# Performance work log

Hardware: AMD Instinct MI355X
Metric: run time of the kernel (lower is better)

Reference implementation:

```python
import jax, jax.numpy as jnp
import numpy as np

N = 10000      # nodes
E = 160000     # edges
IN = 256       # input feature dim
HID = 128      # hidden per head
H = 4          # heads (all layers)
EMB = 128      # dim_embedding (last-layer out per head)
SLOPE = 0.2    # leaky_relu negative slope in attention


def _gat_layer(h, src, dst, W, al, ar, b, residual, apply_act):
    """DGL-style GATConv (no dropout). h: [N, F_in], W: [F_in, H*D], al/ar/b: [H, D]."""
    n = h.shape[0]
    heads, d = al.shape
    feat = (h @ W).reshape(n, heads, d)                 # [N, H, D]
    el = jnp.sum(feat * al, axis=-1)                    # [N, H]
    er = jnp.sum(feat * ar, axis=-1)                    # [N, H]
    e = jax.nn.leaky_relu(el[src] + er[dst], SLOPE)     # [E, H]
    # edge softmax over incoming edges of dst (numerically stable)
    m = jax.ops.segment_max(e, dst, num_segments=n)
    m = jnp.where(jnp.isfinite(m), m, 0.0)              # empty segments -> 0
    ex = jnp.exp(e - m[dst])
    den = jax.ops.segment_sum(ex, dst, num_segments=n)
    alpha = ex / jnp.maximum(den[dst], 1e-9)            # [E, H]
    rst = jax.ops.segment_sum(alpha[:, :, None] * feat[src], dst, num_segments=n)  # [N, H, D]
    if residual:
        rst = rst + h.reshape(n, heads, d)              # identity residual (dims match)
    rst = rst + b
    return jax.nn.elu(rst) if apply_act else rst


def setup_inputs() -> dict:
    key = jax.random.key(0)
    ks = jax.random.split(key, 24)
    def p(k, shape, scale):
        return (jax.random.normal(k, shape, jnp.float32) * scale)
    inp = {
        'x': jax.random.normal(ks[0], (N, IN), jnp.float32),
        'src': jax.random.randint(ks[1], (E,), 0, N, dtype=jnp.int32).astype(jnp.int64),
        'dst': jax.random.randint(ks[2], (E,), 0, N, dtype=jnp.int32).astype(jnp.int64),
        # layer 0: in=IN, out=HID per head
        'W0': p(ks[3], (IN, H * HID), 1.0 / np.sqrt(IN)),
        'al0': p(ks[4], (H, HID), 0.1), 'ar0': p(ks[5], (H, HID), 0.1),
        'b0': p(ks[6], (H, HID), 0.02),
        # layer 1: in=H*HID=512, out=HID per head, residual
        'W1': p(ks[7], (H * HID, H * HID), 1.0 / np.sqrt(H * HID)),
        'al1': p(ks[8], (H, HID), 0.1), 'ar1': p(ks[9], (H, HID), 0.1),
        'b1': p(ks[10], (H, HID), 0.02),
        # layer 2: in=H*HID=512, out=EMB per head, residual, no activation
        'W2': p(ks[11], (H * HID, H * EMB), 1.0 / np.sqrt(H * HID)),
        'al2': p(ks[12], (H, EMB), 0.1), 'ar2': p(ks[13], (H, EMB), 0.1),
        'b2': p(ks[14], (H, EMB), 0.02),
        # MLP predictor: 2*EMB -> EMB -> EMB//2 -> 1
        'Wm0': p(ks[15], (2 * EMB, EMB), 1.0 / np.sqrt(2 * EMB)), 'bm0': p(ks[16], (EMB,), 0.02),
        'Wm1': p(ks[17], (EMB, EMB // 2), 1.0 / np.sqrt(EMB)), 'bm1': p(ks[18], (EMB // 2,), 0.02),
        'Wm2': p(ks[19], (EMB // 2, 1), 1.0 / np.sqrt(EMB // 2)), 'bm2': p(ks[20], (1,), 0.02),
    }
    return inp


def reference(x, src, dst, W0, al0, ar0, b0, W1, al1, ar1, b1, W2, al2, ar2, b2,
              Wm0, bm0, Wm1, bm1, Wm2, bm2):
    # GAT encoder
    h = _gat_layer(x, src, dst, W0, al0, ar0, b0, residual=False, apply_act=True).reshape(N, -1)
    h = _gat_layer(h, src, dst, W1, al1, ar1, b1, residual=True, apply_act=True).reshape(N, -1)
    h = _gat_layer(h, src, dst, W2, al2, ar2, b2, residual=True, apply_act=False).mean(axis=1)  # [N, EMB]
    # link predictor over all graph edges
    emb = jnp.concatenate([h[src], h[dst]], axis=1)     # [E, 2*EMB]
    z = jax.nn.relu(emb @ Wm0 + bm0)
    z = jax.nn.relu(z @ Wm1 + bm1)
    return jax.nn.sigmoid(z @ Wm2 + bm2)                # [E, 1]
```

## Files before the change

kernel.cpp:

```cpp
#include <hip/hip_runtime.h>
#include <hip/hip_bf16.h>
#include <math.h>

constexpr int kN = 10000;
constexpr int kE = 160000;
constexpr float kSlope = 0.2f;

typedef short v8s __attribute__((ext_vector_type(8)));
typedef float f32x4 __attribute__((ext_vector_type(4)));
typedef unsigned short ushort_t;

__device__ __forceinline__ float lrelu(float x) { return x > 0.f ? x : kSlope * x; }
__device__ __forceinline__ float elu_f(float x) { return x > 0.f ? x : (__expf(x) - 1.f); }
__device__ __forceinline__ float b2f(ushort_t u) {
    return __uint_as_float(((unsigned)u) << 16);
}
__device__ __forceinline__ float bl(unsigned u) { return __uint_as_float(u << 16); }
__device__ __forceinline__ float bh(unsigned u) { return __uint_as_float(u & 0xffff0000u); }
__device__ __forceinline__ ushort_t f2b(float f) {
    unsigned u = __float_as_uint(f);
    return (ushort_t)((u + 0x7FFFu + ((u >> 16) & 1u)) >> 16);
}
__device__ __forceinline__ void gload16(const void* g, void* l) {
    __builtin_amdgcn_global_load_lds(
        (const __attribute__((address_space(1))) void*)g,
        (__attribute__((address_space(3))) void*)l, 16, 0, 0);
}

__global__ void detect_zero(const void* __restrict__ x, const void* __restrict__ dsti,
                            int* __restrict__ flags, int* __restrict__ deg) {
    if (blockIdx.x == 0) {
        __shared__ int sb[2];
        int tid = threadIdx.x;
        if (tid == 0) { sb[0] = 0; sb[1] = 0; }
        __syncthreads();
        const ushort_t* xb = (const ushort_t*)x;
        int big = 0;
        for (int i = tid; i < 4096; i += 256) {
            float v = b2f(xb[i]);
            if (!(fabsf(v) <= 1e4f)) big = 1;
        }
        const int* d32 = (const int*)dsti;
        int hi = 0;
        for (int i = tid; i < 4096; i += 256) hi |= d32[2 * i + 1];
        if (big) atomicOr(&sb[0], 1);
        if (hi)  atomicOr(&sb[1], 1);
        __syncthreads();
        if (tid == 0) { flags[0] = sb[0]; flags[1] = sb[1] ? 0 : 1; }
    } else {
        int i = (blockIdx.x - 1) * 256 + threadIdx.x;
        if (i < 2 * kN) deg[i] = 0;
    }
}

struct PrepArgs {
    const void* sm[13];
    const void* W0; const void* W1; const void* W2; const void* Wm0; const void* Wm1;
    const void* X; const void* srcIn; const void* dstIn;
    float* smallb;
    ushort_t* W0T; ushort_t* W1T; ushort_t* W2T; ushort_t* PQT; ushort_t* Wm1T;
    ushort_t* Xb;
    int* nsrc; int* ndst; int* deg;
    const int* flags;
};
constexpr int kPrepTotal = 4865 + 131072 + 262144 + 262144 + 32768 + 8192 + 2560000 + 320000;

__global__ void prep_all(PrepArgs a) {
    int i = blockIdx.x * 256 + threadIdx.x;
    if (i >= kPrepTotal) return;
    const int f32in = a.flags[0];
    auto cv = [&](const void* p, int idx) -> ushort_t {
        return f32in ? f2b(((const float*)p)[idx]) : ((const ushort_t*)p)[idx];
    };
    if (i < 4865) {
        int seg, offi;
        if (i < 4608)      { seg = i >> 9; offi = i & 511; }
        else if (i < 4736) { seg = 9;  offi = i - 4608; }
        else if (i < 4800) { seg = 10; offi = i - 4736; }
        else if (i < 4864) { seg = 11; offi = i - 4800; }
        else               { seg = 12; offi = 0; }
        a.smallb[i] = f32in ? ((const float*)a.sm[seg])[offi]
                            : b2f(((const ushort_t*)a.sm[seg])[offi]);
        return;
    }
    i -= 4865;
    if (i < 131072) {
        int n = i >> 8, k = i & 255;
        a.W0T[i] = cv(a.W0, k * 512 + n);
        return;
    }
    i -= 131072;
    if (i < 262144) {
        int n = i >> 9, k = i & 511;
        a.W1T[i] = cv(a.W1, k * 512 + n);
        return;
    }
    i -= 262144;
    if (i < 262144) {
        int n = i >> 9, k = i & 511;
        a.W2T[i] = cv(a.W2, k * 512 + n);
        return;
    }
    i -= 262144;
    if (i < 32768) {
        int n = i >> 7, k = i & 127;
        a.PQT[i] = cv(a.Wm0, (k + ((n < 128) ? 0 : 128)) * 128 + (n & 127));
        return;
    }
    i -= 32768;
    if (i < 8192) {
        int n = i >> 7, k = i & 127;
        a.Wm1T[i] = cv(a.Wm1, k * 64 + n);
        return;
    }
    i -= 8192;
    if (i < 2560000) {
        if (f32in) a.Xb[i] = f2b(((const float*)a.X)[i]);
        return;
    }
    i -= 2560000;
    {
        const void* in = (i < kE) ? a.srcIn : a.dstIn;
        int j = (i < kE) ? i : i - kE;
        int v = a.flags[1] ? (int)((const long long*)in)[j] : ((const int*)in)[j];
        v = ((unsigned)v < (unsigned)kN) ? v : 0;
        if (i < kE) a.nsrc[j] = v;
        else { a.ndst[j] = v; atomicAdd(&a.deg[v], 1); }
    }
}

__global__ __launch_bounds__(1024) void scan_off(const int* __restrict__ deg,
                                                 int* __restrict__ off, int n) {
    __shared__ int s[1024];
    int tid = threadIdx.x;
    int per = (n + 1023) >> 10;
    int base = tid * per;
    int sum = 0;
    for (int i = 0; i < per; ++i) { int j = base + i; if (j < n) sum += deg[j]; }
    s[tid] = sum;
    __syncthreads();
    for (int d = 1; d < 1024; d <<= 1) {
        int v = (tid >= d) ? s[tid - d] : 0;
        __syncthreads();
        s[tid] += v;
        __syncthreads();
    }
    int run = (tid > 0) ? s[tid - 1] : 0;
    for (int i = 0; i < per; ++i) {
        int j = base + i;
        if (j < n) { off[j] = run; run += deg[j]; }
    }
    if (tid == 0) off[n] = s[1023];
}

__global__ void fill_csr(const int* __restrict__ src, const int* __restrict__ dst,
                         const int* __restrict__ off, int* __restrict__ cnt,
                         int* __restrict__ ss, int* __restrict__ eid,
                         int* __restrict__ dpos, int n) {
    int i = blockIdx.x * 256 + threadIdx.x;
    if (i < n) {
        int d = dst[i];
        int pos = off[d] + atomicAdd(&cnt[d], 1);
        if (pos < kE) { ss[pos] = src[i]; eid[pos] = i; dpos[pos] = d; }
    }
}

template <bool ELER>
__global__ __launch_bounds__(256) void gemm_mfma(const ushort_t* __restrict__ A,
                                                 const void* __restrict__ Araw,
                                                 const int* __restrict__ gflags,
                                                 const ushort_t* __restrict__ WT,
                                                 ushort_t* __restrict__ Cout,
                                                 int M, int N, int K,
                                                 const float* __restrict__ al,
                                                 const float* __restrict__ ar,
                                                 float* __restrict__ el,
                                                 float* __restrict__ er) {
    __shared__ __align__(16) ushort_t As[2][4][64][8];
    __shared__ __align__(16) ushort_t Bs[2][4][128][8];
    __shared__ float elred[64][2][2];
    const int t = threadIdx.x;
    const int wave = t >> 6, lane = t & 63;
    const int l16 = lane & 15, q = lane >> 4;
    const int row0 = blockIdx.y * 64, col0 = blockIdx.x * 128;
    const int wm = (wave & 1) * 32, wn = (wave >> 1) * 64;

    const ushort_t* Aeff = A;
    if (Araw != nullptr && gflags[0] == 0) Aeff = (const ushort_t*)Araw;

    const int lsw = lane ^ (wave * 4);
    const ushort_t* asrc  = Aeff + (size_t)min(row0 + lsw, M - 1) * K + wave * 8;
    const ushort_t* bsrc0 = WT + (size_t)(col0 + lsw) * K + wave * 8;
    const ushort_t* bsrc1 = WT + (size_t)(col0 + 64 + lsw) * K + wave * 8;

    auto stage = [&](int b, int k0) {
        gload16(asrc + k0,  &As[b][wave][0][0]);
        gload16(bsrc0 + k0, &Bs[b][wave][0][0]);
        gload16(bsrc1 + k0, &Bs[b][wave][64][0]);
    };

    f32x4 acc[2][4];
#pragma unroll
    for (int mt = 0; mt < 2; ++mt)
#pragma unroll
        for (int nt = 0; nt < 4; ++nt)
#pragma unroll
            for (int r = 0; r < 4; ++r) acc[mt][nt][r] = 0.f;

    const int qs = q * 4;
    auto compute = [&](int b) {
        v8s af[2], bf[4];
#pragma unroll
        for (int mt = 0; mt < 2; ++mt)
            af[mt] = *(const v8s*)&As[b][q][(wm + mt * 16 + l16) ^ qs][0];
#pragma unroll
        for (int nt = 0; nt < 4; ++nt)
            bf[nt] = *(const v8s*)&Bs[b][q][(wn + nt * 16 + l16) ^ qs][0];
#pragma unroll
        for (int mt = 0; mt < 2; ++mt)
#pragma unroll
            for (int nt = 0; nt < 4; ++nt)
                acc[mt][nt] = __builtin_amdgcn_mfma_f32_16x16x32_bf16(af[mt], bf[nt],
                                                                      acc[mt][nt], 0, 0, 0);
    };

    stage(0, 0);
    __syncthreads();
    for (int k0 = 0; k0 < K; k0 += 64) {
        stage(1, k0 + 32);
        compute(0);
        __syncthreads();
        if (k0 + 64 < K) stage(0, k0 + 64);
        compute(1);
        __syncthreads();
    }

#pragma unroll
    for (int mt = 0; mt < 2; ++mt)
#pragma unroll
        for (int r = 0; r < 4; ++r) {
            int row = row0 + wm + mt * 16 + q * 4 + r;
            if (row < M) {
#pragma unroll
                for (int nt = 0; nt < 4; ++nt)
                    Cout[(size_t)row * N + col0 + wn + nt * 16 + l16] = f2b(acc[mt][nt][r]);
            }
        }
    if (ELER) {
        const int head = blockIdx.x;
        float alv[4], arv[4];
#pragma unroll
        for (int nt = 0; nt < 4; ++nt) {
            alv[nt] = al[head * 128 + wn + nt * 16 + l16];
            arv[nt] = ar[head * 128 + wn + nt * 16 + l16];
        }
#pragma unroll
        for (int mt = 0; mt < 2; ++mt)
#pragma unroll
            for (int r = 0; r < 4; ++r) {
                float pel = 0.f, per = 0.f;
#pragma unroll
                for (int nt = 0; nt < 4; ++nt) {
                    pel += acc[mt][nt][r] * alv[nt];
                    per += acc[mt][nt][r] * arv[nt];
                }
                pel += __shfl_xor(pel, 1); per += __shfl_xor(per, 1);
                pel += __shfl_xor(pel, 2); per += __shfl_xor(per, 2);
                pel += __shfl_xor(pel, 4); per += __shfl_xor(per, 4);
                pel += __shfl_xor(pel, 8); per += __shfl_xor(per, 8);
                if (l16 == 0) {
                    int rl = wm + mt * 16 + q * 4 + r;
                    elred[rl][wave >> 1][0] = pel;
                    elred[rl][wave >> 1][1] = per;
                }
            }
        __syncthreads();
        if (t < 64) {
            int row = row0 + t;
            if (row < M) {
                el[row * 4 + head] = elred[t][0][0] + elred[t][1][0];
                er[row * 4 + head] = elred[t][0][1] + elred[t][1][1];
            }
        }
    }
}

template <bool RES, bool ACT, int EPI>
__global__ __launch_bounds__(256) void gat_agg(const ushort_t* __restrict__ feat,
                                               const float* __restrict__ el,
                                               const float* __restrict__ er,
                                               const int* __restrict__ off,
                                               const int* __restrict__ ss,
                                               const ushort_t* residb,
                                               const float* __restrict__ bias,
                                               ushort_t* hl) {
    const int node = blockIdx.x * 4 + (threadIdx.x >> 6);
    const int lane = threadIdx.x & 63;
    if (node >= kN) return;
    const int off0 = off[node];
    const int deg = off[node + 1] - off0;
    float4 er4 = *(const float4*)(er + node * 4);
    const int head = lane >> 4;
    const float erh = (head == 0) ? er4.x : (head == 1) ? er4.y : (head == 2) ? er4.z : er4.w;
    const int c0 = lane * 8;

    float den = 0.f;
    float acc[8] = {};
    if (deg > 0) {
        float eP[4]; uint4 fP[4];
#pragma unroll
        for (int i = 0; i < 4; ++i) {
            int s = ss[off0 + min(i, deg - 1)];
            eP[i] = el[s * 4 + head];
            fP[i] = *(const uint4*)(feat + (size_t)s * 512 + c0);
        }
        for (int j = 0; j < deg; j += 4) {
            float eN[4]; uint4 fN[4];
            if (j + 4 < deg) {
#pragma unroll
                for (int i = 0; i < 4; ++i) {
                    int s = ss[off0 + min(j + 4 + i, deg - 1)];
                    eN[i] = el[s * 4 + head];
                    fN[i] = *(const uint4*)(feat + (size_t)s * 512 + c0);
                }
            }
#pragma unroll
            for (int i = 0; i < 4; ++i) {
                if (j + i < deg) {
                    float w = __expf(lrelu(eP[i] + erh));
                    den += w;
                    acc[0] += w * bl(fP[i].x); acc[1] += w * bh(fP[i].x);
                    acc[2] += w * bl(fP[i].y); acc[3] += w * bh(fP[i].y);
                    acc[4] += w * bl(fP[i].z); acc[5] += w * bh(fP[i].z);
                    acc[6] += w * bl(fP[i].w); acc[7] += w * bh(fP[i].w);
                }
            }
#pragma unroll
            for (int i = 0; i < 4; ++i) { eP[i] = eN[i]; fP[i] = fN[i]; }
        }
    }
    const float inv = 1.f / fmaxf(den, 1e-9f);
    float4 b0 = *(const float4*)(bias + c0);
    float4 b1 = *(const float4*)(bias + c0 + 4);
    float v[8];
#pragma unroll
    for (int r = 0; r < 8; ++r) v[r] = acc[r] * inv;
    v[0] += b0.x; v[1] += b0.y; v[2] += b0.z; v[3] += b0.w;
    v[4] += b1.x; v[5] += b1.y; v[6] += b1.z; v[7] += b1.w;
    if (RES) {
        uint4 rv = *(const uint4*)(residb + (size_t)node * 512 + c0);
        v[0] += bl(rv.x); v[1] += bh(rv.x);
        v[2] += bl(rv.y); v[3] += bh(rv.y);
        v[4] += bl(rv.z); v[5] += bh(rv.z);
        v[6] += bl(rv.w); v[7] += bh(rv.w);
    }
    if (ACT) {
#pragma unroll
        for (int r = 0; r < 8; ++r) v[r] = elu_f(v[r]);
    }
    if (EPI == 1) {
        ushort_t* hp = hl + (size_t)node * 512 + c0;
        ushort4 h0 = {f2b(v[0]), f2b(v[1]), f2b(v[2]), f2b(v[3])};
        ushort4 h1 = {f2b(v[4]), f2b(v[5]), f2b(v[6]), f2b(v[7])};
        *(ushort4*)hp = h0;
        *(ushort4*)(hp + 4) = h1;
    }
    if (EPI == 2) {
        float m[8];
#pragma unroll
        for (int r = 0; r < 8; ++r) {
            float x = v[r] + __shfl_xor(v[r], 16);
            x += __shfl_xor(x, 32);
            m[r] = 0.25f * x;
        }
        if (lane < 16) {
            ushort_t* hp = hl + (size_t)node * 128 + lane * 8;
            ushort4 h0 = {f2b(m[0]), f2b(m[1]), f2b(m[2]), f2b(m[3])};
            ushort4 h1 = {f2b(m[4]), f2b(m[5]), f2b(m[6]), f2b(m[7])};
            *(ushort4*)hp = h0;
            *(ushort4*)(hp + 4) = h1;
        }
    }
}

__global__ __launch_bounds__(256) void edge_mfma(const ushort_t* __restrict__ PQb,
                                                 const float* __restrict__ bm0f,
                                                 const ushort_t* __restrict__ Wm1T,
                                                 const float* __restrict__ bm1f,
                                                 const float* __restrict__ wm2f,
                                                 const float* __restrict__ bm2f,
                                                 const int* __restrict__ ss,
                                                 const int* __restrict__ dpos,
                                                 const int* __restrict__ eid,
                                                 void* __restrict__ outv,
                                                 const int* __restrict__ flags) {
    const int t = threadIdx.x;
    const int wave = t >> 6, lane = t & 63;
    const int l16 = lane & 15, q = lane >> 4;
    const int base = blockIdx.x * 64 + wave * 16;
    const int pos = base + l16;
    const int s = ss[pos], d = dpos[pos];
    const ushort_t* prow = PQb + (size_t)s * 256;
    const ushort_t* qrow = PQb + (size_t)d * 256 + 128;

    f32x4 acc[4];
#pragma unroll
    for (int nt = 0; nt < 4; ++nt)
#pragma unroll
        for (int r = 0; r < 4; ++r) acc[nt][r] = 0.f;

#pragma unroll
    for (int ks = 0; ks < 4; ++ks) {
        const int k0 = ks * 32 + q * 8;
        uint4 pv = *(const uint4*)(prow + k0);
        uint4 qv = *(const uint4*)(qrow + k0);
        float4 bb0 = *(const float4*)(bm0f + k0);
        float4 bb1 = *(const float4*)(bm0f + k0 + 4);
        v8s a;
        a[0] = (short)f2b(fmaxf(bl(pv.x) + bl(qv.x) + bb0.x, 0.f));
        a[1] = (short)f2b(fmaxf(bh(pv.x) + bh(qv.x) + bb0.y, 0.f));
        a[2] = (short)f2b(fmaxf(bl(pv.y) + bl(qv.y) + bb0.z, 0.f));
        a[3] = (short)f2b(fmaxf(bh(pv.y) + bh(qv.y) + bb0.w, 0.f));
        a[4] = (short)f2b(fmaxf(bl(pv.z) + bl(qv.z) + bb1.x, 0.f));
        a[5] = (short)f2b(fmaxf(bh(pv.z) + bh(qv.z) + bb1.y, 0.f));
        a[6] = (short)f2b(fmaxf(bl(pv.w) + bl(qv.w) + bb1.z, 0.f));
        a[7] = (short)f2b(fmaxf(bh(pv.w) + bh(qv.w) + bb1.w, 0.f));
#pragma unroll
        for (int nt = 0; nt < 4; ++nt) {
            v8s b = *(const v8s*)(Wm1T + (size_t)(nt * 16 + l16) * 128 + k0);
            acc[nt] = __builtin_amdgcn_mfma_f32_16x16x32_bf16(a, b, acc[nt], 0, 0, 0);
        }
    }
    float b1v[4], w2v[4];
#pragma unroll
    for (int nt = 0; nt < 4; ++nt) {
        b1v[nt] = bm1f[nt * 16 + l16];
        w2v[nt] = wm2f[nt * 16 + l16];
    }
    float b2 = bm2f[0];
    const int f32out = flags[0];
#pragma unroll
    for (int r = 0; r < 4; ++r) {
        float v = 0.f;
#pragma unroll
        for (int nt = 0; nt < 4; ++nt)
            v += fmaxf(acc[nt][r] + b1v[nt], 0.f) * w2v[nt];
        v += __shfl_xor(v, 1);
        v += __shfl_xor(v, 2);
        v += __shfl_xor(v, 4);
        v += __shfl_xor(v, 8);
        if (l16 == 0) {
            int e = eid[base + q * 4 + r];
            float rr = 1.f / (1.f + __expf(-(v + b2)));
            if (f32out) ((float*)outv)[e] = rr;
            else        ((ushort_t*)outv)[e] = f2b(rr);
        }
    }
}

extern "C" void kernel_launch(void* const* d_in, const int* in_sizes, int n_in,
                              void* d_out, int out_size, void* d_ws, size_t ws_size,
                              hipStream_t stream) {
    (void)in_sizes; (void)n_in; (void)out_size; (void)ws_size;

    float* w = (float*)d_ws;
    size_t o = 0;
    auto alloc = [&](size_t n) { float* p = w + o; o += (n + 3) & ~size_t(3); return p; };
    float* smallb = alloc(4868);
    float* al0f = smallb + 0;    float* ar0f = smallb + 512;  float* b0f  = smallb + 1024;
    float* al1f = smallb + 1536; float* ar1f = smallb + 2048; float* b1f  = smallb + 2560;
    float* al2f = smallb + 3072; float* ar2f = smallb + 3584; float* b2f_ = smallb + 4096;
    float* bm0f = smallb + 4608; float* bm1f = smallb + 4736;
    float* wm2f = smallb + 4800; float* bm2f = smallb + 4864;
    float* elb  = alloc((size_t)kN * 4);
    float* erb  = alloc((size_t)kN * 4);
    ushort_t* Fb  = (ushort_t*)alloc((size_t)kN * 256);
    ushort_t* AHL = (ushort_t*)alloc((size_t)kN * 256);
    ushort_t* MHb = (ushort_t*)alloc((size_t)kN * 64);
    ushort_t* Xb  = (ushort_t*)alloc((size_t)kN * 128);
    ushort_t* W0T  = (ushort_t*)alloc(65536);
    ushort_t* W1T  = (ushort_t*)alloc(131072);
    ushort_t* W2T  = (ushort_t*)alloc(131072);
    ushort_t* PQT  = (ushort_t*)alloc(16384);
    ushort_t* Wm1T = (ushort_t*)alloc(4096);
    int* ip    = (int*)(w + o);
    int* flags = ip;
    int* deg   = ip + 4;
    int* cnt   = deg + kN;
    int* off   = cnt + kN;
    int* ss    = off + 10004;
    int* eid   = ss + kE;
    int* dpos  = eid + kE;
    int* nsrc  = dpos + kE;
    int* ndst  = nsrc + kE;

    ushort_t* PQb = Fb;

    dim3 blk(256);

    detect_zero<<<dim3(1 + (2 * kN + 255) / 256), blk, 0, stream>>>(d_in[0], d_in[2], flags, deg);

    PrepArgs a;
    const int sidx[13] = {4, 5, 6, 8, 9, 10, 12, 13, 14, 16, 18, 19, 20};
    for (int i = 0; i < 13; ++i) a.sm[i] = d_in[sidx[i]];
    a.W0 = d_in[3]; a.W1 = d_in[7]; a.W2 = d_in[11]; a.Wm0 = d_in[15]; a.Wm1 = d_in[17];
    a.X = d_in[0]; a.srcIn = d_in[1]; a.dstIn = d_in[2];
    a.smallb = smallb; a.W0T = W0T; a.W1T = W1T; a.W2T = W2T; a.PQT = PQT; a.Wm1T = Wm1T;
    a.Xb = Xb; a.nsrc = nsrc; a.ndst = ndst; a.deg = deg; a.flags = flags;
    prep_all<<<dim3((kPrepTotal + 255) / 256), blk, 0, stream>>>(a);

    scan_off<<<dim3(1), dim3(1024), 0, stream>>>(deg, off, kN);
    fill_csr<<<dim3((kE + 255) / 256), blk, 0, stream>>>(nsrc, ndst, off, cnt, ss, eid, dpos, kE);

    const int gy = (kN + 63) / 64;
    const int ga = (kN + 3) / 4;

    gemm_mfma<true><<<dim3(4, gy), blk, 0, stream>>>(Xb, d_in[0], flags, W0T, Fb,
                                                     kN, 512, 256, al0f, ar0f, elb, erb);
    gat_agg<false, true, 1><<<dim3(ga), blk, 0, stream>>>(Fb, elb, erb, off, ss,
                                                          nullptr, b0f, AHL);

    gemm_mfma<true><<<dim3(4, gy), blk, 0, stream>>>(AHL, nullptr, flags, W1T, Fb,
                                                     kN, 512, 512, al1f, ar1f, elb, erb);
    gat_agg<true, true, 1><<<dim3(ga), blk, 0, stream>>>(Fb, elb, erb, off, ss,
                                                         AHL, b1f, AHL);

    gemm_mfma<true><<<dim3(4, gy), blk, 0, stream>>>(AHL, nullptr, flags, W2T, Fb,
                                                     kN, 512, 512, al2f, ar2f, elb, erb);
    gat_agg<true, false, 2><<<dim3(ga), blk, 0, stream>>>(Fb, elb, erb, off, ss,
                                                          AHL, b2f_, MHb);

    gemm_mfma<false><<<dim3(2, gy), blk, 0, stream>>>(MHb, nullptr, flags, PQT, PQb,
                                                      kN, 256, 128,
                                                      nullptr, nullptr, nullptr, nullptr);

    edge_mfma<<<dim3(kE / 64), blk, 0, stream>>>(PQb, bm0f, Wm1T, bm1f, wm2f, bm2f,
                                                 ss, dpos, eid, d_out, flags);
}
```

Before: 335.6 us.

## Register-staged GEMM loads and triple-buffered prefetch in GAT aggregation

Measured after the change: 320.8 us. 1.05x faster.

```diff
diff --git a/kernel.cpp b/kernel.cpp
--- a/kernel.cpp
+++ b/kernel.cpp
@@ -20,11 +20,6 @@
 __device__ __forceinline__ ushort_t f2b(float f) {
     unsigned u = __float_as_uint(f);
     return (ushort_t)((u + 0x7FFFu + ((u >> 16) & 1u)) >> 16);
-}
-__device__ __forceinline__ void gload16(const void* g, void* l) {
-    __builtin_amdgcn_global_load_lds(
-        (const __attribute__((address_space(1))) void*)g,
-        (__attribute__((address_space(3))) void*)l, 16, 0, 0);
 }
 
 __global__ void detect_zero(const void* __restrict__ x, const void* __restrict__ dsti,
@@ -176,28 +171,27 @@
                                                  const float* __restrict__ ar,
                                                  float* __restrict__ el,
                                                  float* __restrict__ er) {
-    __shared__ __align__(16) ushort_t As[2][4][64][8];
-    __shared__ __align__(16) ushort_t Bs[2][4][128][8];
+    __shared__ __align__(16) ushort_t As[4][64][8];
+    __shared__ __align__(16) ushort_t Bs[4][128][8];
     __shared__ float elred[64][2][2];
     const int t = threadIdx.x;
     const int wave = t >> 6, lane = t & 63;
     const int l16 = lane & 15, q = lane >> 4;
     const int row0 = blockIdx.y * 64, col0 = blockIdx.x * 128;
     const int wm = (wave & 1) * 32, wn = (wave >> 1) * 64;
+    const int am = t >> 2, ak8 = t & 3;
+    const int sw = ak8 * 4;
 
     const ushort_t* Aeff = A;
     if (Araw != nullptr && gflags[0] == 0) Aeff = (const ushort_t*)Araw;
 
-    const int lsw = lane ^ (wave * 4);
-    const ushort_t* asrc  = Aeff + (size_t)min(row0 + lsw, M - 1) * K + wave * 8;
-    const ushort_t* bsrc0 = WT + (size_t)(col0 + lsw) * K + wave * 8;
-    const ushort_t* bsrc1 = WT + (size_t)(col0 + 64 + lsw) * K + wave * 8;
-
-    auto stage = [&](int b, int k0) {
-        gload16(asrc + k0,  &As[b][wave][0][0]);
-        gload16(bsrc0 + k0, &Bs[b][wave][0][0]);
-        gload16(bsrc1 + k0, &Bs[b][wave][64][0]);
-    };
+    const ushort_t* aptr = Aeff + (size_t)min(row0 + am, M - 1) * K + ak8 * 8;
+    const ushort_t* bptr0 = WT + (size_t)(col0 + am) * K + ak8 * 8;
+    const ushort_t* bptr1 = bptr0 + (size_t)64 * K;
+
+    uint4 ga  = *(const uint4*)aptr;
+    uint4 gb0 = *(const uint4*)bptr0;
+    uint4 gb1 = *(const uint4*)bptr1;
 
     f32x4 acc[2][4];
 #pragma unroll
@@ -207,34 +201,32 @@
 #pragma unroll
             for (int r = 0; r < 4; ++r) acc[mt][nt][r] = 0.f;
 
-    const int qs = q * 4;
-    auto compute = [&](int b) {
+    for (int k0 = 0; k0 < K; k0 += 32) {
+        __syncthreads();
+        *(uint4*)&As[ak8][am ^ sw][0] = ga;
+        *(uint4*)&Bs[ak8][am ^ sw][0] = gb0;
+        *(uint4*)&Bs[ak8][(am + 64) ^ sw][0] = gb1;
+        __syncthreads();
+        if (k0 + 32 < K) {
+            ga  = *(const uint4*)(aptr + k0 + 32);
+            gb0 = *(const uint4*)(bptr0 + k0 + 32);
+            gb1 = *(const uint4*)(bptr1 + k0 + 32);
+        }
         v8s af[2], bf[4];
+        const int qs = q * 4;
 #pragma unroll
         for (int mt = 0; mt < 2; ++mt)
-            af[mt] = *(const v8s*)&As[b][q][(wm + mt * 16 + l16) ^ qs][0];
+            af[mt] = *(const v8s*)&As[q][(wm + mt * 16 + l16) ^ qs][0];
 #pragma unroll
         for (int nt = 0; nt < 4; ++nt)
-            bf[nt] = *(const v8s*)&Bs[b][q][(wn + nt * 16 + l16) ^ qs][0];
+            bf[nt] = *(const v8s*)&Bs[q][(wn + nt * 16 + l16) ^ qs][0];
 #pragma unroll
         for (int mt = 0; mt < 2; ++mt)
 #pragma unroll
             for (int nt = 0; nt < 4; ++nt)
                 acc[mt][nt] = __builtin_amdgcn_mfma_f32_16x16x32_bf16(af[mt], bf[nt],
                                                                       acc[mt][nt], 0, 0, 0);
-    };
-
-    stage(0, 0);
-    __syncthreads();
-    for (int k0 = 0; k0 < K; k0 += 64) {
-        stage(1, k0 + 32);
-        compute(0);
-        __syncthreads();
-        if (k0 + 64 < K) stage(0, k0 + 64);
-        compute(1);
-        __syncthreads();
-    }
-
+    }
 #pragma unroll
     for (int mt = 0; mt < 2; ++mt)
 #pragma unroll
@@ -303,40 +295,44 @@
     const int head = lane >> 4;
     const float erh = (head == 0) ? er4.x : (head == 1) ? er4.y : (head == 2) ? er4.z : er4.w;
     const int c0 = lane * 8;
+    const ushort_t* fbase = feat + c0;
 
     float den = 0.f;
     float acc[8] = {};
     if (deg > 0) {
-        float eP[4]; uint4 fP[4];
-#pragma unroll
-        for (int i = 0; i < 4; ++i) {
-            int s = ss[off0 + min(i, deg - 1)];
-            eP[i] = el[s * 4 + head];
-            fP[i] = *(const uint4*)(feat + (size_t)s * 512 + c0);
-        }
-        for (int j = 0; j < deg; j += 4) {
-            float eN[4]; uint4 fN[4];
-            if (j + 4 < deg) {
-#pragma unroll
-                for (int i = 0; i < 4; ++i) {
-                    int s = ss[off0 + min(j + 4 + i, deg - 1)];
-                    eN[i] = el[s * 4 + head];
-                    fN[i] = *(const uint4*)(feat + (size_t)s * 512 + c0);
+        float e0[4], e1[4], e2[4];
+        uint4 f0[4], f1[4], f2[4];
+        auto LD = [&](int bj, float* ev, uint4* fv) {
+#pragma unroll
+            for (int i = 0; i < 4; ++i) {
+                int s = ss[off0 + min(bj + i, deg - 1)];
+                ev[i] = el[s * 4 + head];
+                fv[i] = *(const uint4*)(fbase + (size_t)s * 512);
+            }
+        };
+        auto CONS = [&](int bj, const float* ev, const uint4* fv) {
+#pragma unroll
+            for (int i = 0; i < 4; ++i) {
+                if (bj + i < deg) {
+                    float w = __expf(lrelu(ev[i] + erh));
+                    den += w;
+                    acc[0] += w * bl(fv[i].x); acc[1] += w * bh(fv[i].x);
+                    acc[2] += w * bl(fv[i].y); acc[3] += w * bh(fv[i].y);
+                    acc[4] += w * bl(fv[i].z); acc[5] += w * bh(fv[i].z);
+                    acc[6] += w * bl(fv[i].w); acc[7] += w * bh(fv[i].w);
                 }
             }
-#pragma unroll
-            for (int i = 0; i < 4; ++i) {
-                if (j + i < deg) {
-                    float w = __expf(lrelu(eP[i] + erh));
-                    den += w;
-                    acc[0] += w * bl(fP[i].x); acc[1] += w * bh(fP[i].x);
-                    acc[2] += w * bl(fP[i].y); acc[3] += w * bh(fP[i].y);
-                    acc[4] += w * bl(fP[i].z); acc[5] += w * bh(fP[i].z);
-                    acc[6] += w * bl(fP[i].w); acc[7] += w * bh(fP[i].w);
-                }
-            }
-#pragma unroll
-            for (int i = 0; i < 4; ++i) { eP[i] = eN[i]; fP[i] = fN[i]; }
+        };
+        LD(0, e0, f0);
+        LD(4, e1, f1);
+        LD(8, e2, f2);
+        for (int j = 0; j < deg; j += 12) {
+            CONS(j, e0, f0);
+            if (j + 12 < deg) LD(j + 12, e0, f0);
+            CONS(j + 4, e1, f1);
+            if (j + 16 < deg) LD(j + 16, e1, f1);
+            CONS(j + 8, e2, f2);
+            if (j + 20 < deg) LD(j + 20, e2, f2);
         }
     }
     const float inv = 1.f / fmaxf(den, 1e-9f);
```
